# Performance work log

Measured on AMD Instinct MI355X. Metric: run time of the kernel, lower is better.

## Reference

```python
import jax, jax.numpy as jnp
import numpy as np

N_NODES = 10000
N_EDGES = 640000
IN_FEAT = 128
OUT_FEAT = 128


def setup_inputs() -> dict:
    key = jax.random.key(0)
    ks = jax.random.split(key, 12)
    inp = {
        "h": jax.random.normal(ks[0], (N_NODES, IN_FEAT), dtype=jnp.float32),
        "e": jax.random.uniform(ks[1], (N_EDGES, 1), dtype=jnp.float32),
        "src": jax.random.randint(ks[2], (N_EDGES,), 0, N_NODES, dtype=jnp.int32),
        "dst": jax.random.randint(ks[3], (N_EDGES,), 0, N_NODES, dtype=jnp.int32),
        # Linear params (torch convention: W [out, in], y = x @ W.T + b)
        "Ws_w": jax.random.normal(ks[4], (OUT_FEAT, IN_FEAT), dtype=jnp.float32) * 0.05,
        "Ws_b": jnp.zeros((OUT_FEAT,), dtype=jnp.float32),
        "Wn_w": jax.random.normal(ks[5], (OUT_FEAT, IN_FEAT), dtype=jnp.float32) * 0.05,
        "Wn_b": jnp.zeros((OUT_FEAT,), dtype=jnp.float32),
        "Wu_w": jax.random.normal(ks[6], (OUT_FEAT, IN_FEAT), dtype=jnp.float32) * 0.05,
        "Wu_b": jnp.zeros((OUT_FEAT,), dtype=jnp.float32),
        "lin_w": jax.random.normal(ks[7], (OUT_FEAT, OUT_FEAT), dtype=jnp.float32) * 0.05,
        "lin_b": jnp.zeros((OUT_FEAT,), dtype=jnp.float32),
    }
    return inp


def _mean_agg(msgs, dst, n_nodes):
    # segment-mean to destination nodes; isolated nodes (deg 0) -> 0 (DGL semantics)
    s = jax.ops.segment_sum(msgs, dst, num_segments=n_nodes)
    deg = jax.ops.segment_sum(jnp.ones((msgs.shape[0],), msgs.dtype), dst,
                              num_segments=n_nodes)
    return s / jnp.maximum(deg, 1.0)[:, None]


def reference(h, e, src, dst, Ws_w, Ws_b, Wn_w, Wn_b, Wu_w, Wu_b, lin_w, lin_b):
    n = h.shape[0]
    h_src = h[src]                      # [E, d] gather of source features
    h_p = _mean_agg(h_src * e, dst, n)  # u_mul_e + mean
    h_u = _mean_agg(h_src, dst, n)      # copy_u + mean
    h_total = (h @ Ws_w.T + Ws_b) + (h_p @ Wn_w.T + Wn_b) + (h_u @ Wu_w.T + Wu_b)
    return h_total @ lin_w.T + lin_b
```

## Files before the change

### kernel.cpp

```cpp
#include <hip/hip_runtime.h>
#include <hip/hip_bf16.h>

#define NFEAT 128
#define NPB 8
#define P 256
#define MAXN 10240
#define CAP 128
#define CVT 384
#define NXCD 8

typedef __attribute__((ext_vector_type(8))) short bf16x8;
typedef __attribute__((ext_vector_type(4))) float f32x4;

__device__ __forceinline__ unsigned short f2bf(float f) {
    const unsigned int u = __float_as_uint(f);
    return (unsigned short)((u + 0x7FFFu + ((u >> 16) & 1u)) >> 16);
}
__device__ __forceinline__ float bflo(unsigned int u) {
    return __uint_as_float(u << 16);
}
__device__ __forceinline__ float bfhi(unsigned int u) {
    return __uint_as_float(u & 0xFFFF0000u);
}

__global__ __launch_bounds__(256) void hist_weights(
        const int* __restrict__ dst, unsigned char* __restrict__ hist,
        int n_edges, int n_nodes,
        const float* __restrict__ h, unsigned short* __restrict__ hb,
        const float* __restrict__ Ws, const float* __restrict__ Wn,
        const float* __restrict__ Wu,
        const float* __restrict__ Wsb, const float* __restrict__ Wnb,
        const float* __restrict__ Wub,
        const float* __restrict__ lin, const float* __restrict__ linb,
        unsigned short* __restrict__ Wcatb, float* __restrict__ btot) {
    __shared__ int lh[MAXN];
    __shared__ float cs[NFEAT], cn[NFEAT], cu[NFEAT], bsum[NFEAT];
    const int tid = threadIdx.x;
    if (blockIdx.x < P) {
        const int b = blockIdx.x;
        for (int n = tid; n < n_nodes; n += 256) lh[n] = 0;
        __syncthreads();
        const int per = (n_edges + P - 1) / P;
        const int beg = b * per;
        const int end = min(beg + per, n_edges);
        for (int i = beg + tid * 4; i < end; i += 1024) {
            if (i + 4 <= end) {
                const int4 d4 = *(const int4*)(dst + i);
                atomicAdd(&lh[d4.x], 1);
                atomicAdd(&lh[d4.y], 1);
                atomicAdd(&lh[d4.z], 1);
                atomicAdd(&lh[d4.w], 1);
            } else {
                for (int k = i; k < end; ++k) atomicAdd(&lh[dst[k]], 1);
            }
        }
        __syncthreads();
        unsigned char* hrow = hist + (size_t)b * n_nodes;
        const int n4 = n_nodes >> 2;
        for (int q = tid; q < n4; q += 256) {
            const int n = q * 4;
            const unsigned int v = (unsigned int)(lh[n] & 255)
                                 | ((unsigned int)(lh[n + 1] & 255) << 8)
                                 | ((unsigned int)(lh[n + 2] & 255) << 16)
                                 | ((unsigned int)(lh[n + 3] & 255) << 24);
            ((unsigned int*)hrow)[q] = v;
        }
        for (int n = n4 * 4 + tid; n < n_nodes; n += 256)
            hrow[n] = (unsigned char)lh[n];
    } else if (blockIdx.x < P + NFEAT) {
        const int i = blockIdx.x - P;
        const int o = tid;
        if (o < NFEAT) {
            cs[o] = Ws[o * NFEAT + i];
            cn[o] = Wn[o * NFEAT + i];
            cu[o] = Wu[o * NFEAT + i];
            bsum[o] = Wsb[o] + Wnb[o] + Wub[o];
        }
        __syncthreads();
        if (o < NFEAT) {
            float a1 = 0.f, a2 = 0.f, a3 = 0.f, ab = 0.f;
            #pragma unroll 4
            for (int k = 0; k < NFEAT; ++k) {
                const float l = lin[o * NFEAT + k];
                a1 += l * cs[k];
                a2 += l * cn[k];
                a3 += l * cu[k];
                ab += l * bsum[k];
            }
            const int tn = o >> 4, ncol = o & 15;
            const int kin = i & 31, quad = kin >> 3, j = kin & 7;
            const int tkbase = (i >> 5);
            const float av[3] = {a1, a2, a3};
            #pragma unroll
            for (int s = 0; s < 3; ++s) {
                const int tk = s * 4 + tkbase;
                const size_t idx =
                    ((size_t)(tk * 8 + tn) * 64 + quad * 16 + ncol) * 8 + j;
                Wcatb[idx] = f2bf(av[s]);
            }
            if (i == 0) btot[o] = ab + linb[o];
        }
    } else {
        const int b = blockIdx.x - P - NFEAT;
        const size_t total4 = (size_t)n_nodes * (NFEAT / 4);
        for (size_t q = (size_t)b * 256 + tid; q < total4; q += (size_t)CVT * 256) {
            const float4 v = *(const float4*)(h + q * 4);
            uint2 o;
            o.x = (unsigned int)f2bf(v.x) | ((unsigned int)f2bf(v.y) << 16);
            o.y = (unsigned int)f2bf(v.z) | ((unsigned int)f2bf(v.w) << 16);
            *(uint2*)(hb + q * 4) = o;
        }
    }
}

__global__ void col_scan(const unsigned char* __restrict__ hist,
                         unsigned char* __restrict__ base,
                         int* __restrict__ cnt, int n_nodes) {
    const int node = blockIdx.x * blockDim.x + threadIdx.x;
    if (node >= n_nodes) return;
    int run = 0;
    #pragma unroll 8
    for (int b = 0; b < P; ++b) {
        const int h = hist[(size_t)b * n_nodes + node];
        base[(size_t)b * n_nodes + node] = (unsigned char)run;
        run += h;
    }
    cnt[node] = run;
}

__global__ __launch_bounds__(256) void scatter_sliced(
        const int* __restrict__ src, const int* __restrict__ dst,
        const float* __restrict__ e, const unsigned char* __restrict__ base,
        int2* __restrict__ eidx, int n_edges, int n_nodes) {
    __shared__ int lh[(MAXN + NXCD - 1) / NXCD];
    const int tid = threadIdx.x;
    const int r = blockIdx.x & (NXCD - 1);
    const int s = blockIdx.x >> 3;
    const int NPR = (n_nodes + NXCD - 1) / NXCD;
    const int nbeg = r * NPR;
    const int nloc = min(nbeg + NPR, n_nodes) - nbeg;
    for (int n = tid; n < nloc; n += 256) {
        const int g = nbeg + n;
        lh[n] = g * CAP + (int)base[(size_t)s * n_nodes + g];
    }
    __syncthreads();
    const int per = (n_edges + P - 1) / P;
    const int beg = s * per;
    const int end = min(beg + per, n_edges);
    for (int i = beg + tid * 4; i < end; i += 1024) {
        if (i + 4 <= end) {
            const int4 d4 = *(const int4*)(dst + i);
            const int4 s4 = *(const int4*)(src + i);
            const float4 e4 = *(const float4*)(e + i);
            const unsigned l0 = (unsigned)(d4.x - nbeg);
            const unsigned l1 = (unsigned)(d4.y - nbeg);
            const unsigned l2 = (unsigned)(d4.z - nbeg);
            const unsigned l3 = (unsigned)(d4.w - nbeg);
            if (l0 < (unsigned)nloc) {
                const int p = atomicAdd(&lh[l0], 1);
                if (p < (d4.x + 1) * CAP) eidx[p] = make_int2(s4.x, __float_as_int(e4.x));
            }
            if (l1 < (unsigned)nloc) {
                const int p = atomicAdd(&lh[l1], 1);
                if (p < (d4.y + 1) * CAP) eidx[p] = make_int2(s4.y, __float_as_int(e4.y));
            }
            if (l2 < (unsigned)nloc) {
                const int p = atomicAdd(&lh[l2], 1);
                if (p < (d4.z + 1) * CAP) eidx[p] = make_int2(s4.z, __float_as_int(e4.z));
            }
            if (l3 < (unsigned)nloc) {
                const int p = atomicAdd(&lh[l3], 1);
                if (p < (d4.w + 1) * CAP) eidx[p] = make_int2(s4.w, __float_as_int(e4.w));
            }
        } else {
            for (int k = i; k < end; ++k) {
                const int d = dst[k];
                const unsigned dl = (unsigned)(d - nbeg);
                if (dl < (unsigned)nloc) {
                    const int pos = atomicAdd(&lh[dl], 1);
                    if (pos < (d + 1) * CAP)
                        eidx[pos] = make_int2(src[k], __float_as_int(e[k]));
                }
            }
        }
    }
}

__global__ __launch_bounds__(256, 4) void agg_gemm(
        const float* __restrict__ h, const unsigned short* __restrict__ hb,
        const int2* __restrict__ eidx,
        const int* __restrict__ cnt, const unsigned short* __restrict__ Wcatb,
        const float* __restrict__ btot, float* __restrict__ out, int n_nodes) {
    __shared__ unsigned short Xsb[3][NPB][NFEAT];
    __shared__ int2 se[NPB][CAP];
    __shared__ int scnt[NPB];
    const int tid = threadIdx.x;
    const int n0 = blockIdx.x * NPB;

    if (tid < NPB) scnt[tid] = (n0 + tid < n_nodes) ? cnt[n0 + tid] : 0;
    __syncthreads();

    for (int i = tid; i < NPB * CAP; i += 256) {
        const int ln = i >> 7;
        const int k  = i & (CAP - 1);
        if (k < min(scnt[ln], CAP)) se[ln][k] = eidx[(size_t)(n0 + ln) * CAP + k];
    }
    {
        const int i = tid;
        const int n = i >> 5;
        const int c4 = i & 31;
        const int gn = n0 + n;
        float4 v = make_float4(0.f, 0.f, 0.f, 0.f);
        if (gn < n_nodes) v = *(const float4*)(h + (size_t)gn * NFEAT + c4 * 4);
        uint2 pk;
        pk.x = (unsigned int)f2bf(v.x) | ((unsigned int)f2bf(v.y) << 16);
        pk.y = (unsigned int)f2bf(v.z) | ((unsigned int)f2bf(v.w) << 16);
        *(uint2*)(&Xsb[0][n][c4 * 4]) = pk;
    }
    __syncthreads();

    {
        const int qw   = tid >> 4;
        const int ql   = tid & 15;
        const int ln   = qw >> 1;
        const int half = qw & 1;
        const int n  = scnt[ln];
        const int nl = min(n, CAP);
        const unsigned short* hbp = hb + ql * 8;
        float su[8] = {0.f,0.f,0.f,0.f,0.f,0.f,0.f,0.f};
        float sp[8] = {0.f,0.f,0.f,0.f,0.f,0.f,0.f,0.f};
        int j = half;
        for (; j + 14 < nl; j += 16) {
            int2 E[8];
            #pragma unroll
            for (int q = 0; q < 8; ++q) E[q] = se[ln][j + 2 * q];
            uint4 H[8];
            #pragma unroll
            for (int q = 0; q < 8; ++q)
                H[q] = *(const uint4*)(hbp + (size_t)E[q].x * NFEAT);
            #pragma unroll
            for (int q = 0; q < 8; ++q) {
                const float v = __int_as_float(E[q].y);
                const float h0 = bflo(H[q].x), h1 = bfhi(H[q].x);
                const float h2 = bflo(H[q].y), h3 = bfhi(H[q].y);
                const float h4 = bflo(H[q].z), h5 = bfhi(H[q].z);
                const float h6 = bflo(H[q].w), h7 = bfhi(H[q].w);
                su[0] += h0; su[1] += h1; su[2] += h2; su[3] += h3;
                su[4] += h4; su[5] += h5; su[6] += h6; su[7] += h7;
                sp[0] += v * h0; sp[1] += v * h1; sp[2] += v * h2; sp[3] += v * h3;
                sp[4] += v * h4; sp[5] += v * h5; sp[6] += v * h6; sp[7] += v * h7;
            }
        }
        for (; j < nl; j += 2) {
            const int2 e0 = se[ln][j];
            const uint4 Hv = *(const uint4*)(hbp + (size_t)e0.x * NFEAT);
            const float v0 = __int_as_float(e0.y);
            const float h0 = bflo(Hv.x), h1 = bfhi(Hv.x);
            const float h2 = bflo(Hv.y), h3 = bfhi(Hv.y);
            const float h4 = bflo(Hv.z), h5 = bfhi(Hv.z);
            const float h6 = bflo(Hv.w), h7 = bfhi(Hv.w);
            su[0] += h0; su[1] += h1; su[2] += h2; su[3] += h3;
            su[4] += h4; su[5] += h5; su[6] += h6; su[7] += h7;
            sp[0] += v0 * h0; sp[1] += v0 * h1; sp[2] += v0 * h2; sp[3] += v0 * h3;
            sp[4] += v0 * h4; sp[5] += v0 * h5; sp[6] += v0 * h6; sp[7] += v0 * h7;
        }
        #pragma unroll
        for (int k = 0; k < 8; ++k) {
            su[k] += __shfl_xor(su[k], 16);
            sp[k] += __shfl_xor(sp[k], 16);
        }
        if (half == 0) {
            const float inv = 1.0f / fmaxf((float)n, 1.0f);
            uint4 a;
            a.x = (unsigned int)f2bf(sp[0] * inv) | ((unsigned int)f2bf(sp[1] * inv) << 16);
            a.y = (unsigned int)f2bf(sp[2] * inv) | ((unsigned int)f2bf(sp[3] * inv) << 16);
            a.z = (unsigned int)f2bf(sp[4] * inv) | ((unsigned int)f2bf(sp[5] * inv) << 16);
            a.w = (unsigned int)f2bf(sp[6] * inv) | ((unsigned int)f2bf(sp[7] * inv) << 16);
            *(uint4*)(&Xsb[1][ln][ql * 8]) = a;
            a.x = (unsigned int)f2bf(su[0] * inv) | ((unsigned int)f2bf(su[1] * inv) << 16);
            a.y = (unsigned int)f2bf(su[2] * inv) | ((unsigned int)f2bf(su[3] * inv) << 16);
            a.z = (unsigned int)f2bf(su[4] * inv) | ((unsigned int)f2bf(su[5] * inv) << 16);
            a.w = (unsigned int)f2bf(su[6] * inv) | ((unsigned int)f2bf(su[7] * inv) << 16);
            *(uint4*)(&Xsb[2][ln][ql * 8]) = a;
        }
    }
    __syncthreads();

    {
        const int wv   = tid >> 6;
        const int lane = tid & 63;
        const int mrow = lane & 15;
        const int quad = lane >> 4;
        const int tn0  = wv * 2;
        f32x4 acc0 = {0.f, 0.f, 0.f, 0.f};
        f32x4 acc1 = {0.f, 0.f, 0.f, 0.f};
        const bf16x8* Wb = (const bf16x8*)Wcatb;
        #pragma unroll
        for (int tk = 0; tk < 12; ++tk) {
            const int s  = tk >> 2;
            const int kb = (tk & 3) * 32 + quad * 8;
            const bf16x8 a  = *(const bf16x8*)(&Xsb[s][mrow & 7][kb]);
            const bf16x8 b0 = Wb[(size_t)(tk * 8 + tn0) * 64 + lane];
            const bf16x8 b1 = Wb[(size_t)(tk * 8 + tn0 + 1) * 64 + lane];
            acc0 = __builtin_amdgcn_mfma_f32_16x16x32_bf16(a, b0, acc0, 0, 0, 0);
            acc1 = __builtin_amdgcn_mfma_f32_16x16x32_bf16(a, b1, acc1, 0, 0, 0);
        }
        const int c0 = tn0 * 16 + mrow;
        const int c1 = (tn0 + 1) * 16 + mrow;
        const float bt0 = btot[c0];
        const float bt1 = btot[c1];
        #pragma unroll
        for (int r = 0; r < 4; ++r) {
            const int row = quad * 4 + r;
            const int gn = n0 + row;
            if (row < NPB && gn < n_nodes) {
                out[(size_t)gn * NFEAT + c0] = acc0[r] + bt0;
                out[(size_t)gn * NFEAT + c1] = acc1[r] + bt1;
            }
        }
    }
}

extern "C" void kernel_launch(void* const* d_in, const int* in_sizes, int n_in,
                              void* d_out, int out_size, void* d_ws, size_t ws_size,
                              hipStream_t stream) {
    const float* h     = (const float*)d_in[0];
    const float* e     = (const float*)d_in[1];
    const int*   src   = (const int*)d_in[2];
    const int*   dst   = (const int*)d_in[3];
    const float* Ws_w  = (const float*)d_in[4];
    const float* Ws_b  = (const float*)d_in[5];
    const float* Wn_w  = (const float*)d_in[6];
    const float* Wn_b  = (const float*)d_in[7];
    const float* Wu_w  = (const float*)d_in[8];
    const float* Wu_b  = (const float*)d_in[9];
    const float* lin_w = (const float*)d_in[10];
    const float* lin_b = (const float*)d_in[11];
    float* out = (float*)d_out;

    const int n_nodes = in_sizes[0] / NFEAT;
    const int n_edges = in_sizes[2];

    char* ws = (char*)d_ws;
    unsigned short* Wcatb = (unsigned short*)ws;  ws += 3 * NFEAT * NFEAT * 2;
    float* btot = (float*)ws;            ws += NFEAT * 4;
    int2*  eidx = (int2*)ws;             ws += (size_t)n_nodes * CAP * 8;
    int*   cnt  = (int*)ws;              ws += n_nodes * 4;
    unsigned short* hb = (unsigned short*)ws;  ws += (size_t)n_nodes * NFEAT * 2;
    unsigned char* hist = (unsigned char*)ws;  ws += (size_t)P * n_nodes;
    unsigned char* base = (unsigned char*)ws;  ws += (size_t)P * n_nodes;

    hist_weights<<<P + NFEAT + CVT, 256, 0, stream>>>(
        dst, hist, n_edges, n_nodes, h, hb,
        Ws_w, Wn_w, Wu_w, Ws_b, Wn_b, Wu_b, lin_w, lin_b, Wcatb, btot);

    col_scan<<<(n_nodes + 255) / 256, 256, 0, stream>>>(hist, base, cnt, n_nodes);

    scatter_sliced<<<P * NXCD, 256, 0, stream>>>(src, dst, e, base, eidx,
                                                 n_edges, n_nodes);

    const int n_blocks = (n_nodes + NPB - 1) / NPB;
    agg_gemm<<<n_blocks, 256, 0, stream>>>(h, hb, eidx, cnt, Wcatb, btot,
                                           out, n_nodes);
}
```

Before: 136.6 us.

## Fuse column scan into scatter kernel and halve edge slice count

Removes the separate col_scan launch. Each scatter block now computes its own per-slice base offsets by summing the histogram rows of earlier slices, and the last slice writes the per-node counts. The slice count drops from 256 to 128 to shrink the redundant prefix reads and the histogram buffer. The cost is extra redundant histogram reads per block and fewer, longer slices in the histogram and scatter phases. NPR is hardcoded to 1280, which assumes n_nodes is at most 10240.

```diff
diff --git a/kernel.cpp b/kernel.cpp
--- a/kernel.cpp
+++ b/kernel.cpp
@@ -3,11 +3,12 @@
 
 #define NFEAT 128
 #define NPB 8
-#define P 256
+#define PB 128
 #define MAXN 10240
 #define CAP 128
 #define CVT 384
 #define NXCD 8
+#define NPR 1280
 
 typedef __attribute__((ext_vector_type(8))) short bf16x8;
 typedef __attribute__((ext_vector_type(4))) float f32x4;
@@ -36,11 +37,11 @@
     __shared__ int lh[MAXN];
     __shared__ float cs[NFEAT], cn[NFEAT], cu[NFEAT], bsum[NFEAT];
     const int tid = threadIdx.x;
-    if (blockIdx.x < P) {
+    if (blockIdx.x < PB) {
         const int b = blockIdx.x;
         for (int n = tid; n < n_nodes; n += 256) lh[n] = 0;
         __syncthreads();
-        const int per = (n_edges + P - 1) / P;
+        const int per = (n_edges + PB - 1) / PB;
         const int beg = b * per;
         const int end = min(beg + per, n_edges);
         for (int i = beg + tid * 4; i < end; i += 1024) {
@@ -67,8 +68,8 @@
         }
         for (int n = n4 * 4 + tid; n < n_nodes; n += 256)
             hrow[n] = (unsigned char)lh[n];
-    } else if (blockIdx.x < P + NFEAT) {
-        const int i = blockIdx.x - P;
+    } else if (blockIdx.x < PB + NFEAT) {
+        const int i = blockIdx.x - PB;
         const int o = tid;
         if (o < NFEAT) {
             cs[o] = Ws[o * NFEAT + i];
@@ -101,7 +102,7 @@
             if (i == 0) btot[o] = ab + linb[o];
         }
     } else {
-        const int b = blockIdx.x - P - NFEAT;
+        const int b = blockIdx.x - PB - NFEAT;
         const size_t total4 = (size_t)n_nodes * (NFEAT / 4);
         for (size_t q = (size_t)b * 256 + tid; q < total4; q += (size_t)CVT * 256) {
             const float4 v = *(const float4*)(h + q * 4);
@@ -113,38 +114,52 @@
     }
 }
 
-__global__ void col_scan(const unsigned char* __restrict__ hist,
-                         unsigned char* __restrict__ base,
-                         int* __restrict__ cnt, int n_nodes) {
-    const int node = blockIdx.x * blockDim.x + threadIdx.x;
-    if (node >= n_nodes) return;
-    int run = 0;
-    #pragma unroll 8
-    for (int b = 0; b < P; ++b) {
-        const int h = hist[(size_t)b * n_nodes + node];
-        base[(size_t)b * n_nodes + node] = (unsigned char)run;
-        run += h;
-    }
-    cnt[node] = run;
-}
-
-__global__ __launch_bounds__(256) void scatter_sliced(
+__global__ __launch_bounds__(256) void scatter_selfbase(
         const int* __restrict__ src, const int* __restrict__ dst,
-        const float* __restrict__ e, const unsigned char* __restrict__ base,
-        int2* __restrict__ eidx, int n_edges, int n_nodes) {
-    __shared__ int lh[(MAXN + NXCD - 1) / NXCD];
+        const float* __restrict__ e, const unsigned char* __restrict__ hist,
+        int2* __restrict__ eidx, int* __restrict__ cnt,
+        int n_edges, int n_nodes) {
+    __shared__ int lh[NPR];
     const int tid = threadIdx.x;
     const int r = blockIdx.x & (NXCD - 1);
     const int s = blockIdx.x >> 3;
-    const int NPR = (n_nodes + NXCD - 1) / NXCD;
     const int nbeg = r * NPR;
     const int nloc = min(nbeg + NPR, n_nodes) - nbeg;
-    for (int n = tid; n < nloc; n += 256) {
-        const int g = nbeg + n;
-        lh[n] = g * CAP + (int)base[(size_t)s * n_nodes + g];
+    if (nloc > 0) {
+        const int nq = nloc >> 2;
+        for (int q = tid; q < nq; q += 256) {
+            const unsigned char* hp = hist + nbeg + q * 4;
+            int r0 = 0, r1 = 0, r2 = 0, r3 = 0;
+            int b = 0;
+            for (; b + 8 <= s; b += 8) {
+                uchar4 v[8];
+                #pragma unroll
+                for (int u = 0; u < 8; ++u)
+                    v[u] = *(const uchar4*)(hp + (size_t)(b + u) * n_nodes);
+                #pragma unroll
+                for (int u = 0; u < 8; ++u) {
+                    r0 += v[u].x; r1 += v[u].y; r2 += v[u].z; r3 += v[u].w;
+                }
+            }
+            for (; b < s; ++b) {
+                const uchar4 v = *(const uchar4*)(hp + (size_t)b * n_nodes);
+                r0 += v.x; r1 += v.y; r2 += v.z; r3 += v.w;
+            }
+            const int g = nbeg + q * 4;
+            lh[q * 4 + 0] = (g + 0) * CAP + r0;
+            lh[q * 4 + 1] = (g + 1) * CAP + r1;
+            lh[q * 4 + 2] = (g + 2) * CAP + r2;
+            lh[q * 4 + 3] = (g + 3) * CAP + r3;
+        }
+        for (int n = nq * 4 + tid; n < nloc; n += 256) {
+            int run = 0;
+            for (int b = 0; b < s; ++b)
+                run += hist[(size_t)b * n_nodes + nbeg + n];
+            lh[n] = (nbeg + n) * CAP + run;
+        }
     }
     __syncthreads();
-    const int per = (n_edges + P - 1) / P;
+    const int per = (n_edges + PB - 1) / PB;
     const int beg = s * per;
     const int end = min(beg + per, n_edges);
     for (int i = beg + tid * 4; i < end; i += 1024) {
@@ -183,6 +198,11 @@
                 }
             }
         }
+    }
+    if (s == PB - 1) {
+        __syncthreads();
+        for (int n = tid; n < nloc; n += 256)
+            cnt[nbeg + n] = lh[n] - (nbeg + n) * CAP;
     }
 }
 
@@ -347,17 +367,14 @@
     int2*  eidx = (int2*)ws;             ws += (size_t)n_nodes * CAP * 8;
     int*   cnt  = (int*)ws;              ws += n_nodes * 4;
     unsigned short* hb = (unsigned short*)ws;  ws += (size_t)n_nodes * NFEAT * 2;
-    unsigned char* hist = (unsigned char*)ws;  ws += (size_t)P * n_nodes;
-    unsigned char* base = (unsigned char*)ws;  ws += (size_t)P * n_nodes;
-
-    hist_weights<<<P + NFEAT + CVT, 256, 0, stream>>>(
+    unsigned char* hist = (unsigned char*)ws;  ws += (size_t)PB * n_nodes;
+
+    hist_weights<<<PB + NFEAT + CVT, 256, 0, stream>>>(
         dst, hist, n_edges, n_nodes, h, hb,
         Ws_w, Wn_w, Wu_w, Ws_b, Wn_b, Wu_b, lin_w, lin_b, Wcatb, btot);
 
-    col_scan<<<(n_nodes + 255) / 256, 256, 0, stream>>>(hist, base, cnt, n_nodes);
-
-    scatter_sliced<<<P * NXCD, 256, 0, stream>>>(src, dst, e, base, eidx,
-                                                 n_edges, n_nodes);
+    scatter_selfbase<<<PB * NXCD, 256, 0, stream>>>(src, dst, e, hist, eidx,
+                                                    cnt, n_edges, n_nodes);
 
     const int n_blocks = (n_nodes + NPB - 1) / NPB;
     agg_gemm<<<n_blocks, 256, 0, stream>>>(h, hb, eidx, cnt, Wcatb, btot,
```

Result: faster. 131.6 us (-3.6%).
